# Performance work log

Hardware: AMD Instinct MI355X
Metric: run time of the kernel (lower is better)

Reference implementation:

```python
import jax, jax.numpy as jnp
import numpy as np

V, E, HD, T = 50000, 300, 512, 9   # vocab, embed_dim, hidden_dim, tagset
H = HD // 2                         # per-direction LSTM hidden
B, S = 64, 512


def _uniform(key, shape, k):
    return jax.random.uniform(key, shape, jnp.float32, -k, k)


def setup_inputs() -> dict:
    key = jax.random.key(0)
    ks = jax.random.split(key, 16)
    klstm = 1.0 / np.sqrt(H)
    kout = 1.0 / np.sqrt(HD)
    embed = jax.random.normal(ks[0], (V, E), jnp.float32) * 0.1
    embed = embed.at[0].set(0.0)  # padding_idx=0
    inp = {
        'sentence': jax.random.randint(ks[1], (B, S), 1, V),
        'tags': jax.random.randint(ks[2], (B, S), 0, T),
        'embed': embed,
        'wih_f': _uniform(ks[3], (4 * H, E), klstm),
        'whh_f': _uniform(ks[4], (4 * H, H), klstm),
        'bih_f': _uniform(ks[5], (4 * H,), klstm),
        'bhh_f': _uniform(ks[6], (4 * H,), klstm),
        'wih_b': _uniform(ks[7], (4 * H, E), klstm),
        'whh_b': _uniform(ks[8], (4 * H, H), klstm),
        'bih_b': _uniform(ks[9], (4 * H,), klstm),
        'bhh_b': _uniform(ks[10], (4 * H,), klstm),
        'w_out': _uniform(ks[11], (T, HD), kout),
        'b_out': _uniform(ks[12], (T,), kout),
        'start_trans': _uniform(ks[13], (T,), 0.1),
        'end_trans': _uniform(ks[14], (T,), 0.1),
        'trans': _uniform(ks[15], (T, T), 0.1),
    }
    # contiguous left-aligned mask with random lengths (mask[:,0]==1 as torchcrf requires)
    lengths = jax.random.randint(jax.random.fold_in(key, 99), (B,), S // 2, S + 1)
    inp['mask'] = (jnp.arange(S)[None, :] < lengths[:, None]).astype(jnp.int32)
    return inp


def _lstm(x, wih, whh, bih, bhh):
    # x: [S,B,E] -> hidden states [S,B,H]; gate order i,f,g,o (PyTorch)
    b = x.shape[1]
    def step(carry, xt):
        h, c = carry
        g = xt @ wih.T + h @ whh.T + (bih + bhh)
        i, f, gg, o = jnp.split(g, 4, axis=-1)
        c = jax.nn.sigmoid(f) * c + jax.nn.sigmoid(i) * jnp.tanh(gg)
        h = jax.nn.sigmoid(o) * jnp.tanh(c)
        return (h, c), h
    init = (jnp.zeros((b, H), x.dtype), jnp.zeros((b, H), x.dtype))
    _, hs = jax.lax.scan(step, init, x)
    return hs


def _forward(sentence, tags, mask, embed, wih_f, whh_f, bih_f, bhh_f,
             wih_b, whh_b, bih_b, bhh_b, w_out, b_out,
             start_trans, end_trans, trans):
    # dropout in eval mode -> identity
    x = embed[sentence].transpose(1, 0, 2)                # [S,B,E]
    hf = _lstm(x, wih_f, whh_f, bih_f, bhh_f)             # [S,B,H]
    hb = _lstm(x[::-1], wih_b, whh_b, bih_b, bhh_b)[::-1]  # [S,B,H]
    hcat = jnp.concatenate([hf, hb], axis=-1)             # [S,B,HD]
    emis = hcat @ w_out.T + b_out                         # [S,B,T]

    mask_t = mask.T.astype(bool)                          # [S,B]
    tags_t = tags.T                                       # [S,B]
    bar = jnp.arange(tags.shape[0])

    # --- numerator: gold path score ---
    score = start_trans[tags_t[0]] + emis[0, bar, tags_t[0]]
    tr_sc = trans[tags_t[:-1], tags_t[1:]]                # [S-1,B]
    em_sc = jnp.take_along_axis(emis[1:], tags_t[1:][..., None], axis=-1)[..., 0]
    score = score + ((tr_sc + em_sc) * mask_t[1:].astype(emis.dtype)).sum(0)
    lengths = mask.astype(jnp.int32).sum(1)
    last_tags = tags[bar, lengths - 1]
    score = score + end_trans[last_tags]

    # --- denominator: forward algorithm (logsumexp DP over tags) ---
    alpha0 = start_trans[None, :] + emis[0]               # [B,T]
    def step(alpha, inp):
        em_i, m_i = inp
        nxt = jax.nn.logsumexp(alpha[:, :, None] + trans[None] + em_i[:, None, :], axis=1)
        return jnp.where(m_i[:, None], nxt, alpha), None
    alpha, _ = jax.lax.scan(step, alpha0, (emis[1:], mask_t[1:]))
    logZ = jax.nn.logsumexp(alpha + end_trans[None, :], axis=1)

    llh = score - logZ
    return -llh.mean()  # torchcrf reduction='mean', negated


def reference(sentence, tags, mask, embed, wih_f, whh_f, bih_f, bhh_f,
              wih_b, whh_b, bih_b, bhh_b, w_out, b_out,
              start_trans, end_trans, trans):
    return _forward(sentence, tags, mask, embed, wih_f, whh_f, bih_f, bhh_f,
                    wih_b, whh_b, bih_b, bhh_b, w_out, b_out,
                    start_trans, end_trans, trans)
```

## Files before the change

kernel.cpp:

```cpp
#include <hip/hip_runtime.h>
#include <hip/hip_bf16.h>
#include <stdint.h>

#define EDIM 300
#define KP   320
#define HDIM 256
#define G4H  1024
#define NB   2048
#define TAGS 9
#define BATCH 64
#define SEQ  512
#define MROWS (SEQ*BATCH)

typedef _Float16 f16;
typedef _Float16 half2_t __attribute__((ext_vector_type(2)));
typedef _Float16 half8_t __attribute__((ext_vector_type(8)));
typedef float    floatx4 __attribute__((ext_vector_type(4)));
typedef uint32_t u32x4   __attribute__((ext_vector_type(4)));

__device__ __forceinline__ float fast_sigmoid(float x) {
    return __builtin_amdgcn_rcpf(1.f + __expf(-x));
}
__device__ __forceinline__ float fast_tanh(float x) {
    return 1.f - 2.f*__builtin_amdgcn_rcpf(__expf(2.f*x) + 1.f);
}

__global__ void k_pack_wih(const float* __restrict__ wih_f, const float* __restrict__ wih_b,
                           const float* __restrict__ bih_f, const float* __restrict__ bhh_f,
                           const float* __restrict__ bih_b, const float* __restrict__ bhh_b,
                           f16* __restrict__ wpack, float* __restrict__ bias2) {
    int n = blockIdx.x;
    const float* src = (n < G4H) ? (wih_f + (long)n*EDIM) : (wih_b + (long)(n-G4H)*EDIM);
    for (int k = threadIdx.x; k < KP; k += 64)
        wpack[(long)n*KP + k] = (k < EDIM) ? (f16)src[k] : (f16)0.f;
    if (threadIdx.x == 0)
        bias2[n] = (n < G4H) ? (bih_f[n] + bhh_f[n]) : (bih_b[n-G4H] + bhh_b[n-G4H]);
}

__global__ void k_pack_whh3(const float* __restrict__ whh_f, const float* __restrict__ whh_b,
                            f16* __restrict__ whhp3) {
    int idx = blockIdx.x*256 + threadIdx.x;
    int lane = idx & 63;
    int kf = (idx >> 6) & 7;
    int fr = (idx >> 9) & 15;
    int w  = (idx >> 13) & 3;
    int dir = idx >> 15;
    const float* whh = dir ? whh_b : whh_f;
    int grow = (fr >> 2)*256 + w*64 + (fr & 3)*16 + (lane & 15);
    int k0 = kf*32 + (lane >> 4)*8;
    const float* src = whh + (long)grow*HDIM + k0;
    f16 tmp[8];
    #pragma unroll
    for (int j = 0; j < 8; ++j) tmp[j] = (f16)src[j];
    *(uint4*)(whhp3 + (size_t)idx*8) = *(uint4*)tmp;
}

__global__ void k_gather(const int* __restrict__ sentence, const float* __restrict__ embed,
                         f16* __restrict__ xg) {
    int m = blockIdx.x;
    int t = m >> 6, b = m & 63;
    int tok = sentence[b*SEQ + t];
    const float* row = embed + (long)tok*EDIM;
    for (int e = threadIdx.x; e < KP; e += 64)
        xg[(long)m*KP + e] = (e < EDIM) ? (f16)row[e] : (f16)0.f;
}

__launch_bounds__(256)
__global__ void k_gemm_xproj(const f16* __restrict__ xg, const f16* __restrict__ wpack,
                             const float* __restrict__ bias2, f16* __restrict__ xp5) {
    __shared__ __align__(16) f16 As[128*40];
    __shared__ __align__(16) f16 Bs[128*40];
    int tid = threadIdx.x;
    int bm = blockIdx.x, bn = blockIdx.y;
    int wid = tid >> 6, lane = tid & 63;
    int waveM = wid & 1, waveN = wid >> 1;
    int quad = lane >> 4, mlo = lane & 15;
    floatx4 acc[4][4] = {};
    for (int k0 = 0; k0 < KP; k0 += 32) {
        for (int it = 0; it < 2; ++it) {
            int c = tid + it*256;
            int row = c >> 2, ko = (c & 3)*8;
            *(uint4*)(&As[row*40 + ko]) = *(const uint4*)(&xg[(long)(bm*128+row)*KP + k0 + ko]);
            *(uint4*)(&Bs[row*40 + ko]) = *(const uint4*)(&wpack[(long)(bn*128+row)*KP + k0 + ko]);
        }
        __syncthreads();
        half8_t af[4], bf[4];
        #pragma unroll
        for (int i = 0; i < 4; ++i)
            af[i] = *(const half8_t*)(&As[(waveM*64 + i*16 + mlo)*40 + quad*8]);
        #pragma unroll
        for (int j = 0; j < 4; ++j)
            bf[j] = *(const half8_t*)(&Bs[(waveN*64 + j*16 + mlo)*40 + quad*8]);
        #pragma unroll
        for (int i = 0; i < 4; ++i)
            #pragma unroll
            for (int j = 0; j < 4; ++j)
                acc[i][j] = __builtin_amdgcn_mfma_f32_16x16x32_f16(af[i], bf[j], acc[i][j], 0, 0, 0);
        __syncthreads();
    }
    #pragma unroll
    for (int i = 0; i < 4; ++i)
        #pragma unroll
        for (int j = 0; j < 4; ++j) {
            int col = bn*128 + waveN*64 + j*16 + mlo;
            float bv = bias2[col];
            int dir = col >> 10, grow = col & 1023;
            int gate = grow >> 8, u = grow & 255;
            int rowp = u*4 + gate;
            #pragma unroll
            for (int r = 0; r < 4; ++r) {
                int row = bm*128 + waveM*64 + i*16 + quad*4 + r;
                int t = row >> 6, bb = row & 63;
                int s = dir ? (SEQ-1-t) : t;
                xp5[((size_t)(dir*64 + bb)*512 + s)*1024 + rowp] = (f16)(acc[i][j][r] + bv);
            }
        }
}

#define AFRAG 64
#define VFRAG 32
#define LFRAG 32
__launch_bounds__(256, 1)
__global__ void k_recur(const f16* __restrict__ xp5, const f16* __restrict__ whhp3,
                        f16* __restrict__ hcat) {
    __shared__ __align__(16) uint4 ldsW[4*LFRAG*64];
    __shared__ __align__(16) float gbuf[4][16][16];
    __shared__ __align__(16) f16 hbuf[2][256];
    int dir = blockIdx.x & 1, b = blockIdx.x >> 1;
    int tid = threadIdx.x, w = tid >> 6, lane = tid & 63;
    int q = lane >> 4;
    int v = lane;

    const f16* wbase = whhp3 + (size_t)(dir*4 + w)*131072;
    u32x4 wa[AFRAG], wv[VFRAG];
    #pragma unroll
    for (int f = 0; f < AFRAG; ++f)
        wa[f] = *(const u32x4*)(wbase + ((size_t)f*64 + lane)*8);
    #pragma unroll
    for (int f = 0; f < VFRAG; ++f)
        wv[f] = *(const u32x4*)(wbase + ((size_t)(AFRAG + f)*64 + lane)*8);
    #pragma unroll
    for (int f2 = 0; f2 < LFRAG; ++f2)
        ldsW[(w*LFRAG + f2)*64 + lane] =
            *(const uint4*)(wbase + ((size_t)(AFRAG + VFRAG + f2)*64 + lane)*8);

    if (tid < 128) ((uint32_t*)&hbuf[0][0])[tid] = 0u;

    const f16* xs = xp5 + ((size_t)(dir*64 + b)*512)*1024 + (w*64 + v)*4;
    uint2 xw = *(const uint2*)xs;

    floatx4 zc = {0.f, 0.f, 0.f, 0.f};
    float cc = 0.f;
    __syncthreads();

    for (int s = 0; s < SEQ; ++s) {
        int t = dir ? (SEQ-1-s) : s;
        int sp = (s+1 < SEQ) ? s+1 : s;
        uint2 xn = *(const uint2*)(xs + (size_t)sp*1024);
        floatx4 acc[16];
        const f16* hp = &hbuf[s & 1][0];
        #pragma unroll
        for (int kf = 0; kf < 8; ++kf) {
            half8_t bf = *(const half8_t*)(hp + kf*32 + q*8);
            #pragma unroll
            for (int fr = 0; fr < 16; ++fr) {
                const int f = fr*8 + kf;
                if (kf == 0) {
                    if (f < AFRAG)
                        asm("v_mfma_f32_16x16x32_f16 %0, %1, %2, %3"
                            : "=&v"(acc[fr]) : "a"(wa[f]), "v"(bf), "v"(zc));
                    else if (f < AFRAG + VFRAG)
                        asm("v_mfma_f32_16x16x32_f16 %0, %1, %2, %3"
                            : "=&v"(acc[fr]) : "v"(wv[f - AFRAG]), "v"(bf), "v"(zc));
                    else {
                        half8_t af = *(const half8_t*)((const f16*)&ldsW[(w*LFRAG + (f - AFRAG - VFRAG))*64 + lane]);
                        asm("v_mfma_f32_16x16x32_f16 %0, %1, %2, %3"
                            : "=&v"(acc[fr]) : "v"(af), "v"(bf), "v"(zc));
                    }
                } else {
                    if (f < AFRAG)
                        asm("v_mfma_f32_16x16x32_f16 %0, %1, %2, %0"
                            : "+v"(acc[fr]) : "a"(wa[f]), "v"(bf));
                    else if (f < AFRAG + VFRAG)
                        asm("v_mfma_f32_16x16x32_f16 %0, %1, %2, %0"
                            : "+v"(acc[fr]) : "v"(wv[f - AFRAG]), "v"(bf));
                    else {
                        half8_t af = *(const half8_t*)((const f16*)&ldsW[(w*LFRAG + (f - AFRAG - VFRAG))*64 + lane]);
                        asm("v_mfma_f32_16x16x32_f16 %0, %1, %2, %0"
                            : "+v"(acc[fr]) : "v"(af), "v"(bf));
                    }
                }
            }
        }
        if ((lane & 15) == 0) {
            #pragma unroll
            for (int fr = 0; fr < 16; ++fr)
                *(floatx4*)&gbuf[w][fr][q*4] = acc[fr];
        }
        {
            int sub = v >> 4, rr = v & 15;
            half2_t xif = __builtin_bit_cast(half2_t, xw.x);
            half2_t xgo = __builtin_bit_cast(half2_t, xw.y);
            float pi = gbuf[w][0  + sub][rr] + (float)xif[0];
            float pf = gbuf[w][4  + sub][rr] + (float)xif[1];
            float pg = gbuf[w][8  + sub][rr] + (float)xgo[0];
            float po = gbuf[w][12 + sub][rr] + (float)xgo[1];
            float si = fast_sigmoid(pi), sf = fast_sigmoid(pf);
            float tg = fast_tanh(pg),   so = fast_sigmoid(po);
            cc = __builtin_fmaf(sf, cc, si*tg);
            f16 hh = (f16)(so * fast_tanh(cc));
            hbuf[(s+1) & 1][w*64 + v] = hh;
            hcat[((size_t)t*64 + b)*512 + dir*HDIM + w*64 + v] = hh;
        }
        xw = xn;
        asm volatile("s_waitcnt lgkmcnt(0)" ::: "memory");
        __builtin_amdgcn_s_barrier();
        asm volatile("" ::: "memory");
    }
}

__launch_bounds__(256)
__global__ void k_emis(const f16* __restrict__ hcat, const float* __restrict__ w_out,
                       const float* __restrict__ b_out, float* __restrict__ emis) {
    int r = blockIdx.x*4 + (threadIdx.x >> 6);
    int lane = threadIdx.x & 63;
    float hv[8];
    #pragma unroll
    for (int i = 0; i < 8; ++i) hv[i] = (float)hcat[(long)r*512 + lane + i*64];
    for (int tag = 0; tag < TAGS; ++tag) {
        float acc = 0.f;
        #pragma unroll
        for (int i = 0; i < 8; ++i) acc += hv[i]*w_out[tag*512 + lane + i*64];
        for (int off = 32; off; off >>= 1) acc += __shfl_xor(acc, off);
        if (lane == 0) emis[(long)r*TAGS + tag] = acc + b_out[tag];
    }
}

__launch_bounds__(256)
__global__ void k_crf(const float* __restrict__ emis, const int* __restrict__ tags,
                      const int* __restrict__ mask, const float* __restrict__ start_trans,
                      const float* __restrict__ end_trans, const float* __restrict__ trans,
                      float* __restrict__ out) {
    int b = blockIdx.x*4 + (threadIdx.x >> 6);
    int lane = threadIdx.x & 63;
    int len = 0;
    #pragma unroll
    for (int i = 0; i < 8; ++i) len += mask[b*SEQ + lane + i*64];
    for (int off = 32; off; off >>= 1) len += __shfl_xor(len, off);
    float sc = 0.f;
    for (int i = 0; i < 8; ++i) {
        int t = 1 + lane + i*64;
        if (t < SEQ && mask[b*SEQ + t]) {
            int tp = tags[b*SEQ + t - 1], tc = tags[b*SEQ + t];
            sc += trans[tp*TAGS + tc] + emis[(long)(t*64 + b)*TAGS + tc];
        }
    }
    for (int off = 32; off; off >>= 1) sc += __shfl_xor(sc, off);
    int tag0 = tags[b*SEQ];
    sc += start_trans[tag0] + emis[(long)b*TAGS + tag0];
    sc += end_trans[tags[b*SEQ + len - 1]];
    bool act = lane < TAGS;
    int j = act ? lane : 0;
    float tcol[TAGS];
    #pragma unroll
    for (int i = 0; i < TAGS; ++i) tcol[i] = trans[i*TAGS + j];
    float alpha = act ? (start_trans[j] + emis[(long)b*TAGS + j]) : -1e30f;
    for (int t = 1; t < SEQ; ++t) {
        int mt = mask[b*SEQ + t];
        float em = emis[(long)(t*64 + b)*TAGS + j];
        float v[TAGS], mx = -1e30f;
        #pragma unroll
        for (int i = 0; i < TAGS; ++i) { v[i] = __shfl(alpha, i) + tcol[i]; mx = fmaxf(mx, v[i]); }
        float ss = 0.f;
        #pragma unroll
        for (int i = 0; i < TAGS; ++i) ss += __expf(v[i] - mx);
        float nxt = mx + __logf(ss) + em;
        if (mt && act) alpha = nxt;
    }
    float fv = act ? (alpha + end_trans[j]) : -1e30f;
    float mx = fv;
    for (int off = 32; off; off >>= 1) mx = fmaxf(mx, __shfl_xor(mx, off));
    float ss = act ? __expf(fv - mx) : 0.f;
    for (int off = 32; off; off >>= 1) ss += __shfl_xor(ss, off);
    float logZ = mx + __logf(ss);
    if (lane == 0) atomicAdd(out, (logZ - sc) * (1.0f/BATCH));
}

extern "C" void kernel_launch(void* const* d_in, const int* in_sizes, int n_in,
                              void* d_out, int out_size, void* d_ws, size_t ws_size,
                              hipStream_t stream) {
    const int*   sentence    = (const int*)  d_in[0];
    const int*   tags        = (const int*)  d_in[1];
    const float* embed       = (const float*)d_in[2];
    const float* wih_f       = (const float*)d_in[3];
    const float* whh_f       = (const float*)d_in[4];
    const float* bih_f       = (const float*)d_in[5];
    const float* bhh_f       = (const float*)d_in[6];
    const float* wih_b       = (const float*)d_in[7];
    const float* whh_b       = (const float*)d_in[8];
    const float* bih_b       = (const float*)d_in[9];
    const float* bhh_b       = (const float*)d_in[10];
    const float* w_out       = (const float*)d_in[11];
    const float* b_out       = (const float*)d_in[12];
    const float* start_trans = (const float*)d_in[13];
    const float* end_trans   = (const float*)d_in[14];
    const float* trans       = (const float*)d_in[15];
    const int*   mask        = (const int*)  d_in[16];

    char* ws = (char*)d_ws;
    f16*   xg     = (f16*)ws;   ws += (size_t)MROWS*KP*2;
    f16*   wpack  = (f16*)ws;   ws += (size_t)NB*KP*2;
    float* bias2  = (float*)ws; ws += (size_t)NB*4;
    f16*   whhp3  = (f16*)ws;   ws += (size_t)1024*512*2;
    f16*   xp5    = (f16*)ws;   ws += (size_t)MROWS*NB*2;
    f16*   hcat   = (f16*)ws;   ws += (size_t)MROWS*512*2;
    float* emis   = (float*)ws; ws += (size_t)MROWS*TAGS*4;

    hipLaunchKernelGGL(k_pack_wih, dim3(NB), dim3(64), 0, stream,
                       wih_f, wih_b, bih_f, bhh_f, bih_b, bhh_b, wpack, bias2);
    hipLaunchKernelGGL(k_pack_whh3, dim3(256), dim3(256), 0, stream, whh_f, whh_b, whhp3);
    hipLaunchKernelGGL(k_gather, dim3(MROWS), dim3(64), 0, stream, sentence, embed, xg);
    hipLaunchKernelGGL(k_gemm_xproj, dim3(256,16), dim3(256), 0, stream, xg, wpack, bias2, xp5);
    hipLaunchKernelGGL(k_recur, dim3(128), dim3(256), 0, stream, xp5, whhp3, hcat);
    hipLaunchKernelGGL(k_emis, dim3(MROWS/4), dim3(256), 0, stream, hcat, w_out, b_out, emis);
    hipMemsetAsync(d_out, 0, sizeof(float), stream);
    hipLaunchKernelGGL(k_crf, dim3(BATCH/4), dim3(256), 0, stream,
                       emis, tags, mask, start_trans, end_trans, trans, (float*)d_out);
}
```

Before: 1.268 ms.

## Split LSTM recurrence across eight waves per block instead of four

The recurrent kernel now runs 512 threads (8 waves) per block, each wave owning 32 hidden units (8 MFMA row-fragments) instead of 64 units (16 fragments). The W_hh repack is changed to match, and the register/LDS split of weight fragments is rebalanced (32 in AGPRs, 13 in VGPRs, 19 in LDS). This halves the serial MFMA chain per wave on each timestep, aiming to cut per-step latency of the sequential loop. In exchange it needs a larger barrier across 8 waves, leaves half of each wave's lanes idle in the gate math, and adds register pressure from the launch bound of 2 blocks.

```diff
diff --git a/kernel.cpp b/kernel.cpp
--- a/kernel.cpp
+++ b/kernel.cpp
@@ -37,22 +37,22 @@
         bias2[n] = (n < G4H) ? (bih_f[n] + bhh_f[n]) : (bih_b[n-G4H] + bhh_b[n-G4H]);
 }
 
-__global__ void k_pack_whh3(const float* __restrict__ whh_f, const float* __restrict__ whh_b,
-                            f16* __restrict__ whhp3) {
+__global__ void k_pack_whh2(const float* __restrict__ whh_f, const float* __restrict__ whh_b,
+                            f16* __restrict__ whhp2) {
     int idx = blockIdx.x*256 + threadIdx.x;
     int lane = idx & 63;
     int kf = (idx >> 6) & 7;
-    int fr = (idx >> 9) & 15;
-    int w  = (idx >> 13) & 3;
+    int fr = (idx >> 9) & 7;
+    int w  = (idx >> 12) & 7;
     int dir = idx >> 15;
     const float* whh = dir ? whh_b : whh_f;
-    int grow = (fr >> 2)*256 + w*64 + (fr & 3)*16 + (lane & 15);
+    int grow = (fr >> 1)*256 + w*32 + (fr & 1)*16 + (lane & 15);
     int k0 = kf*32 + (lane >> 4)*8;
     const float* src = whh + (long)grow*HDIM + k0;
     f16 tmp[8];
     #pragma unroll
     for (int j = 0; j < 8; ++j) tmp[j] = (f16)src[j];
-    *(uint4*)(whhp3 + (size_t)idx*8) = *(uint4*)tmp;
+    *(uint4*)(whhp2 + (size_t)idx*8) = *(uint4*)tmp;
 }
 
 __global__ void k_gather(const int* __restrict__ sentence, const float* __restrict__ embed,
@@ -117,37 +117,38 @@
         }
 }
 
-#define AFRAG 64
-#define VFRAG 32
-#define LFRAG 32
-__launch_bounds__(256, 1)
-__global__ void k_recur(const f16* __restrict__ xp5, const f16* __restrict__ whhp3,
+#define NA 32
+#define NV 13
+#define NL 19
+__launch_bounds__(512, 2)
+__global__ void k_recur(const f16* __restrict__ xp5, const f16* __restrict__ whhp2,
                         f16* __restrict__ hcat) {
-    __shared__ __align__(16) uint4 ldsW[4*LFRAG*64];
-    __shared__ __align__(16) float gbuf[4][16][16];
+    __shared__ __align__(16) uint4 ldsW[8*NL*64];
+    __shared__ __align__(16) float gbuf[8][8][16];
     __shared__ __align__(16) f16 hbuf[2][256];
     int dir = blockIdx.x & 1, b = blockIdx.x >> 1;
     int tid = threadIdx.x, w = tid >> 6, lane = tid & 63;
     int q = lane >> 4;
-    int v = lane;
-
-    const f16* wbase = whhp3 + (size_t)(dir*4 + w)*131072;
-    u32x4 wa[AFRAG], wv[VFRAG];
-    #pragma unroll
-    for (int f = 0; f < AFRAG; ++f)
+
+    const f16* wbase = whhp2 + (size_t)(dir*8 + w)*32768;
+    u32x4 wa[NA], wv[NV];
+    #pragma unroll
+    for (int f = 0; f < NA; ++f)
         wa[f] = *(const u32x4*)(wbase + ((size_t)f*64 + lane)*8);
     #pragma unroll
-    for (int f = 0; f < VFRAG; ++f)
-        wv[f] = *(const u32x4*)(wbase + ((size_t)(AFRAG + f)*64 + lane)*8);
-    #pragma unroll
-    for (int f2 = 0; f2 < LFRAG; ++f2)
-        ldsW[(w*LFRAG + f2)*64 + lane] =
-            *(const uint4*)(wbase + ((size_t)(AFRAG + VFRAG + f2)*64 + lane)*8);
+    for (int f = 0; f < NV; ++f)
+        wv[f] = *(const u32x4*)(wbase + ((size_t)(NA + f)*64 + lane)*8);
+    #pragma unroll
+    for (int f2 = 0; f2 < NL; ++f2)
+        ldsW[(w*NL + f2)*64 + lane] =
+            *(const uint4*)(wbase + ((size_t)(NA + NV + f2)*64 + lane)*8);
 
     if (tid < 128) ((uint32_t*)&hbuf[0][0])[tid] = 0u;
 
-    const f16* xs = xp5 + ((size_t)(dir*64 + b)*512)*1024 + (w*64 + v)*4;
-    uint2 xw = *(const uint2*)xs;
+    int u = w*32 + (lane & 31);
+    const f16* xs = xp5 + ((size_t)(dir*64 + b)*512)*1024 + u*4;
+    uint2 xw = {0u, 0u};
+    if ((lane & 63) < 32) xw = *(const uint2*)xs;
 
     floatx4 zc = {0.f, 0.f, 0.f, 0.f};
     float cc = 0.f;
@@ -155,37 +156,40 @@
 
     for (int s = 0; s < SEQ; ++s) {
         int t = dir ? (SEQ-1-s) : s;
-        int sp = (s+1 < SEQ) ? s+1 : s;
-        uint2 xn = *(const uint2*)(xs + (size_t)sp*1024);
-        floatx4 acc[16];
+        uint2 xn = xw;
+        if ((lane & 63) < 32) {
+            int sp = (s+1 < SEQ) ? s+1 : s;
+            xn = *(const uint2*)(xs + (size_t)sp*1024);
+        }
+        floatx4 acc[8];
         const f16* hp = &hbuf[s & 1][0];
         #pragma unroll
         for (int kf = 0; kf < 8; ++kf) {
             half8_t bf = *(const half8_t*)(hp + kf*32 + q*8);
             #pragma unroll
-            for (int fr = 0; fr < 16; ++fr) {
+            for (int fr = 0; fr < 8; ++fr) {
                 const int f = fr*8 + kf;
                 if (kf == 0) {
-                    if (f < AFRAG)
+                    if (f < NA)
                         asm("v_mfma_f32_16x16x32_f16 %0, %1, %2, %3"
                             : "=&v"(acc[fr]) : "a"(wa[f]), "v"(bf), "v"(zc));
-                    else if (f < AFRAG + VFRAG)
+                    else if (f < NA + NV)
                         asm("v_mfma_f32_16x16x32_f16 %0, %1, %2, %3"
-                            : "=&v"(acc[fr]) : "v"(wv[f - AFRAG]), "v"(bf), "v"(zc));
+                            : "=&v"(acc[fr]) : "v"(wv[f - NA]), "v"(bf), "v"(zc));
                     else {
-                        half8_t af = *(const half8_t*)((const f16*)&ldsW[(w*LFRAG + (f - AFRAG - VFRAG))*64 + lane]);
+                        half8_t af = *(const half8_t*)((const f16*)&ldsW[(w*NL + (f - NA - NV))*64 + lane]);
                         asm("v_mfma_f32_16x16x32_f16 %0, %1, %2, %3"
                             : "=&v"(acc[fr]) : "v"(af), "v"(bf), "v"(zc));
                     }
                 } else {
-                    if (f < AFRAG)
+                    if (f < NA)
                         asm("v_mfma_f32_16x16x32_f16 %0, %1, %2, %0"
                             : "+v"(acc[fr]) : "a"(wa[f]), "v"(bf));
-                    else if (f < AFRAG + VFRAG)
+                    else if (f < NA + NV)
                         asm("v_mfma_f32_16x16x32_f16 %0, %1, %2, %0"
-                            : "+v"(acc[fr]) : "v"(wv[f - AFRAG]), "v"(bf));
+                            : "+v"(acc[fr]) : "v"(wv[f - NA]), "v"(bf));
                     else {
-                        half8_t af = *(const half8_t*)((const f16*)&ldsW[(w*LFRAG + (f - AFRAG - VFRAG))*64 + lane]);
+                        half8_t af = *(const half8_t*)((const f16*)&ldsW[(w*NL + (f - NA - NV))*64 + lane]);
                         asm("v_mfma_f32_16x16x32_f16 %0, %1, %2, %0"
                             : "+v"(acc[fr]) : "v"(af), "v"(bf));
                     }
@@ -194,25 +198,25 @@
         }
         if ((lane & 15) == 0) {
             #pragma unroll
-            for (int fr = 0; fr < 16; ++fr)
+            for (int fr = 0; fr < 8; ++fr)
                 *(floatx4*)&gbuf[w][fr][q*4] = acc[fr];
         }
-        {
-            int sub = v >> 4, rr = v & 15;
+        if ((lane & 63) < 32) {
+            int h16 = (lane >> 4) & 1, rr = lane & 15;
             half2_t xif = __builtin_bit_cast(half2_t, xw.x);
             half2_t xgo = __builtin_bit_cast(half2_t, xw.y);
-            float pi = gbuf[w][0  + sub][rr] + (float)xif[0];
-            float pf = gbuf[w][4  + sub][rr] + (float)xif[1];
-            float pg = gbuf[w][8  + sub][rr] + (float)xgo[0];
-            float po = gbuf[w][12 + sub][rr] + (float)xgo[1];
+            float pi = gbuf[w][0 + h16][rr] + (float)xif[0];
+            float pf = gbuf[w][2 + h16][rr] + (float)xif[1];
+            float pg = gbuf[w][4 + h16][rr] + (float)xgo[0];
+            float po = gbuf[w][6 + h16][rr] + (float)xgo[1];
             float si = fast_sigmoid(pi), sf = fast_sigmoid(pf);
             float tg = fast_tanh(pg),   so = fast_sigmoid(po);
             cc = __builtin_fmaf(sf, cc, si*tg);
             f16 hh = (f16)(so * fast_tanh(cc));
-            hbuf[(s+1) & 1][w*64 + v] = hh;
-            hcat[((size_t)t*64 + b)*512 + dir*HDIM + w*64 + v] = hh;
-        }
-        xw = xn;
+            hbuf[(s+1) & 1][u] = hh;
+            hcat[((size_t)t*64 + b)*512 + dir*HDIM + u] = hh;
+            xw = xn;
+        }
         asm volatile("s_waitcnt lgkmcnt(0)" ::: "memory");
         __builtin_amdgcn_s_barrier();
         asm volatile("" ::: "memory");
@@ -311,17 +315,17 @@
     f16*   xg     = (f16*)ws;   ws += (size_t)MROWS*KP*2;
     f16*   wpack  = (f16*)ws;   ws += (size_t)NB*KP*2;
     float* bias2  = (float*)ws; ws += (size_t)NB*4;
-    f16*   whhp3  = (f16*)ws;   ws += (size_t)1024*512*2;
+    f16*   whhp2  = (f16*)ws;   ws += (size_t)1024*512*2;
     f16*   xp5    = (f16*)ws;   ws += (size_t)MROWS*NB*2;
     f16*   hcat   = (f16*)ws;   ws += (size_t)MROWS*512*2;
     float* emis   = (float*)ws; ws += (size_t)MROWS*TAGS*4;
 
     hipLaunchKernelGGL(k_pack_wih, dim3(NB), dim3(64), 0, stream,
                        wih_f, wih_b, bih_f, bhh_f, bih_b, bhh_b, wpack, bias2);
-    hipLaunchKernelGGL(k_pack_whh3, dim3(256), dim3(256), 0, stream, whh_f, whh_b, whhp3);
+    hipLaunchKernelGGL(k_pack_whh2, dim3(256), dim3(256), 0, stream, whh_f, whh_b, whhp2);
     hipLaunchKernelGGL(k_gather, dim3(MROWS), dim3(64), 0, stream, sentence, embed, xg);
     hipLaunchKernelGGL(k_gemm_xproj, dim3(256,16), dim3(256), 0, stream, xg, wpack, bias2, xp5);
-    hipLaunchKernelGGL(k_recur, dim3(128), dim3(256), 0, stream, xp5, whhp3, hcat);
+    hipLaunchKernelGGL(k_recur, dim3(128), dim3(512), 0, stream, xp5, whhp2, hcat);
     hipLaunchKernelGGL(k_emis, dim3(MROWS/4), dim3(256), 0, stream, hcat, w_out, b_out, emis);
     hipMemsetAsync(d_out, 0, sizeof(float), stream);
     hipLaunchKernelGGL(k_crf, dim3(BATCH/4), dim3(256), 0, stream,
```

Result: slower. 1.321 ms (+4.2%).

## Reorder recurrent weight fragments by k-slice and register-prefetch GEMM tiles

Applied to the files above, without the earlier changes.

The recurrent weight pack now orders fragments k-slice-major (kf*16+fr) instead of fr-major, so AGPR-resident fragments cover the early k-slices. The VGPR/LDS split moves from 32/32 to 26/38, which frees vector registers at the cost of more LDS reads per step. In the input-projection GEMM, the next K tile is prefetched into registers before the MFMA work so global load latency can overlap compute. The k_recur loop now assumes every kf==0 fragment lives in AGPRs, and that holds because AFRAG is 64.

```diff
diff --git a/kernel.cpp b/kernel.cpp
--- a/kernel.cpp
+++ b/kernel.cpp
@@ -41,10 +41,11 @@
                             f16* __restrict__ whhp3) {
     int idx = blockIdx.x*256 + threadIdx.x;
     int lane = idx & 63;
-    int kf = (idx >> 6) & 7;
-    int fr = (idx >> 9) & 15;
+    int slot = (idx >> 6) & 127;
     int w  = (idx >> 13) & 3;
     int dir = idx >> 15;
+    int fr = slot & 15;
+    int kf = slot >> 4;
     const float* whh = dir ? whh_b : whh_f;
     int grow = (fr >> 2)*256 + w*64 + (fr & 3)*16 + (lane & 15);
     int k0 = kf*32 + (lane >> 4)*8;
@@ -75,15 +76,27 @@
     int wid = tid >> 6, lane = tid & 63;
     int waveM = wid & 1, waveN = wid >> 1;
     int quad = lane >> 4, mlo = lane & 15;
+    int c0 = tid,        r0 = c0 >> 2, o0 = (c0 & 3)*8;
+    int c1 = tid + 256,  r1 = c1 >> 2, o1 = (c1 & 3)*8;
+    const f16* ag = xg    + (long)(bm*128)*KP;
+    const f16* bg = wpack + (long)(bn*128)*KP;
+    uint4 pa0 = *(const uint4*)(&ag[(long)r0*KP + o0]);
+    uint4 pa1 = *(const uint4*)(&ag[(long)r1*KP + o1]);
+    uint4 pb0 = *(const uint4*)(&bg[(long)r0*KP + o0]);
+    uint4 pb1 = *(const uint4*)(&bg[(long)r1*KP + o1]);
     floatx4 acc[4][4] = {};
     for (int k0 = 0; k0 < KP; k0 += 32) {
-        for (int it = 0; it < 2; ++it) {
-            int c = tid + it*256;
-            int row = c >> 2, ko = (c & 3)*8;
-            *(uint4*)(&As[row*40 + ko]) = *(const uint4*)(&xg[(long)(bm*128+row)*KP + k0 + ko]);
-            *(uint4*)(&Bs[row*40 + ko]) = *(const uint4*)(&wpack[(long)(bn*128+row)*KP + k0 + ko]);
-        }
+        *(uint4*)(&As[r0*40 + o0]) = pa0;
+        *(uint4*)(&As[r1*40 + o1]) = pa1;
+        *(uint4*)(&Bs[r0*40 + o0]) = pb0;
+        *(uint4*)(&Bs[r1*40 + o1]) = pb1;
         __syncthreads();
+        if (k0 + 32 < KP) {
+            pa0 = *(const uint4*)(&ag[(long)r0*KP + k0+32 + o0]);
+            pa1 = *(const uint4*)(&ag[(long)r1*KP + k0+32 + o1]);
+            pb0 = *(const uint4*)(&bg[(long)r0*KP + k0+32 + o0]);
+            pb1 = *(const uint4*)(&bg[(long)r1*KP + k0+32 + o1]);
+        }
         half8_t af[4], bf[4];
         #pragma unroll
         for (int i = 0; i < 4; ++i)
@@ -118,8 +131,8 @@
 }
 
 #define AFRAG 64
-#define VFRAG 32
-#define LFRAG 32
+#define VFRAG 26
+#define LFRAG 38
 __launch_bounds__(256, 1)
 __global__ void k_recur(const f16* __restrict__ xp5, const f16* __restrict__ whhp3,
                         f16* __restrict__ hcat) {
@@ -134,15 +147,15 @@
     const f16* wbase = whhp3 + (size_t)(dir*4 + w)*131072;
     u32x4 wa[AFRAG], wv[VFRAG];
     #pragma unroll
-    for (int f = 0; f < AFRAG; ++f)
-        wa[f] = *(const u32x4*)(wbase + ((size_t)f*64 + lane)*8);
-    #pragma unroll
-    for (int f = 0; f < VFRAG; ++f)
-        wv[f] = *(const u32x4*)(wbase + ((size_t)(AFRAG + f)*64 + lane)*8);
-    #pragma unroll
-    for (int f2 = 0; f2 < LFRAG; ++f2)
-        ldsW[(w*LFRAG + f2)*64 + lane] =
-            *(const uint4*)(wbase + ((size_t)(AFRAG + VFRAG + f2)*64 + lane)*8);
+    for (int g = 0; g < AFRAG; ++g)
+        wa[g] = *(const u32x4*)(wbase + ((size_t)g*64 + lane)*8);
+    #pragma unroll
+    for (int g = 0; g < VFRAG; ++g)
+        wv[g] = *(const u32x4*)(wbase + ((size_t)(AFRAG + g)*64 + lane)*8);
+    #pragma unroll
+    for (int g2 = 0; g2 < LFRAG; ++g2)
+        ldsW[(w*LFRAG + g2)*64 + lane] =
+            *(const uint4*)(wbase + ((size_t)(AFRAG + VFRAG + g2)*64 + lane)*8);
 
     if (tid < 128) ((uint32_t*)&hbuf[0][0])[tid] = 0u;
 
@@ -164,28 +177,19 @@
             half8_t bf = *(const half8_t*)(hp + kf*32 + q*8);
             #pragma unroll
             for (int fr = 0; fr < 16; ++fr) {
-                const int f = fr*8 + kf;
+                const int g = kf*16 + fr;
                 if (kf == 0) {
-                    if (f < AFRAG)
-                        asm("v_mfma_f32_16x16x32_f16 %0, %1, %2, %3"
-                            : "=&v"(acc[fr]) : "a"(wa[f]), "v"(bf), "v"(zc));
-                    else if (f < AFRAG + VFRAG)
-                        asm("v_mfma_f32_16x16x32_f16 %0, %1, %2, %3"
-                            : "=&v"(acc[fr]) : "v"(wv[f - AFRAG]), "v"(bf), "v"(zc));
+                    asm("v_mfma_f32_16x16x32_f16 %0, %1, %2, %3"
+                        : "=&v"(acc[fr]) : "a"(wa[g]), "v"(bf), "v"(zc));
+                } else {
+                    if (g < AFRAG)
+                        asm("v_mfma_f32_16x16x32_f16 %0, %1, %2, %0"
+                            : "+v"(acc[fr]) : "a"(wa[g]), "v"(bf));
+                    else if (g < AFRAG + VFRAG)
+                        asm("v_mfma_f32_16x16x32_f16 %0, %1, %2, %0"
+                            : "+v"(acc[fr]) : "v"(wv[g - AFRAG]), "v"(bf));
                     else {
-                        half8_t af = *(const half8_t*)((const f16*)&ldsW[(w*LFRAG + (f - AFRAG - VFRAG))*64 + lane]);
-                        asm("v_mfma_f32_16x16x32_f16 %0, %1, %2, %3"
-                            : "=&v"(acc[fr]) : "v"(af), "v"(bf), "v"(zc));
-                    }
-                } else {
-                    if (f < AFRAG)
-                        asm("v_mfma_f32_16x16x32_f16 %0, %1, %2, %0"
-                            : "+v"(acc[fr]) : "a"(wa[f]), "v"(bf));
-                    else if (f < AFRAG + VFRAG)
-                        asm("v_mfma_f32_16x16x32_f16 %0, %1, %2, %0"
-                            : "+v"(acc[fr]) : "v"(wv[f - AFRAG]), "v"(bf));
-                    else {
-                        half8_t af = *(const half8_t*)((const f16*)&ldsW[(w*LFRAG + (f - AFRAG - VFRAG))*64 + lane]);
+                        half8_t af = *(const half8_t*)((const f16*)&ldsW[(w*LFRAG + (g - AFRAG - VFRAG))*64 + lane]);
                         asm("v_mfma_f32_16x16x32_f16 %0, %1, %2, %0"
                             : "+v"(acc[fr]) : "v"(af), "v"(bf));
                     }
```

New measurement: 1.286 ms. Within noise of the previous version (+1.4%).
